# Kernel optimization log

Measured on AMD Instinct MI355X. Metric: run time of the kernel, lower is better.

Reference implementation:

```python
import jax, jax.numpy as jnp
import numpy as np

DIM_Q = 512
DIM_K = 512
DIM_V = 512
NUM_HEADS = 8
TEMPERATURE = 0.1
LN_EPS = 1e-5


def setup_inputs() -> dict:
    key = jax.random.key(0)
    ks = jax.random.split(key, 12)
    B, n_q, n_k = 8, 1024, 1024
    s = 0.02
    return {
        "Q": jax.random.normal(ks[0], (B, n_q, DIM_Q), jnp.float32),
        "K": jax.random.normal(ks[1], (B, n_k, DIM_K), jnp.float32),
        "mask": jnp.ones((B, n_k), dtype=bool),
        "Wq": jax.random.normal(ks[2], (DIM_Q, DIM_V), jnp.float32) * s,
        "bq": jnp.zeros((DIM_V,), jnp.float32),
        "Wk": jax.random.normal(ks[3], (DIM_K, DIM_V), jnp.float32) * s,
        "bk": jnp.zeros((DIM_V,), jnp.float32),
        "Wv": jax.random.normal(ks[4], (DIM_K, DIM_V), jnp.float32) * s,
        "bv": jnp.zeros((DIM_V,), jnp.float32),
        "Wo": jax.random.normal(ks[5], (DIM_V, DIM_V), jnp.float32) * s,
        "bo": jnp.zeros((DIM_V,), jnp.float32),
        "gamma": jnp.ones((DIM_V,), jnp.float32),
        "beta": jnp.zeros((DIM_V,), jnp.float32),
    }


def _mab(Q, K, mask, Wq, bq, Wk, bk, Wv, bv, Wo, bo, gamma, beta):
    B, n_q, _ = Q.shape
    n_k = K.shape[1]
    H = NUM_HEADS
    d_head = DIM_V // H
    # projections, split heads: [B, H, n, d_head]
    Qh = (Q @ Wq + bq).reshape(B, n_q, H, d_head).transpose(0, 2, 1, 3)
    Kh = (K @ Wk + bk).reshape(B, n_k, H, d_head).transpose(0, 2, 1, 3)
    Vh = (K @ Wv + bv).reshape(B, n_k, H, d_head).transpose(0, 2, 1, 3)
    scale = 1.0 / (np.sqrt(d_head) * TEMPERATURE)
    A = jnp.einsum("bhqd,bhkd->bhqk", Qh, Kh) * scale
    A = jnp.where(mask[:, None, None, :], A, -jnp.inf)
    A = jax.nn.softmax(A, axis=-1)
    O = jnp.einsum("bhqk,bhkd->bhqd", A, Vh)
    O = O.transpose(0, 2, 1, 3).reshape(B, n_q, DIM_V)
    # fused output FFN + residual + LN
    O = O + jax.nn.relu(O @ Wo + bo)
    mu = jnp.mean(O, axis=-1, keepdims=True)
    var = jnp.var(O, axis=-1, keepdims=True)
    return (O - mu) * jax.lax.rsqrt(var + LN_EPS) * gamma + beta


def reference(Q, K, mask, Wq, bq, Wk, bk, Wv, bv, Wo, bo, gamma, beta):
    return _mab(Q, K, mask, Wq, bq, Wk, bk, Wv, bv, Wo, bo, gamma, beta)
```

## Files before the change

### kernel.cpp

```cpp
#include <hip/hip_runtime.h>

typedef __bf16 bf16;
typedef bf16 bf16x4 __attribute__((ext_vector_type(4)));
typedef bf16 bf16x8 __attribute__((ext_vector_type(8)));
typedef float floatx4 __attribute__((ext_vector_type(4)));

#define NB 8
#define NQ 1024
#define NK 1024
#define DIM 512
#define NH 8
#define DH 64

__device__ __forceinline__ void async16(const void* g, void* l) {
    __builtin_amdgcn_global_load_lds(
        (const __attribute__((address_space(1))) unsigned int*)(unsigned long long)(g),
        (__attribute__((address_space(3))) unsigned int*)(unsigned long long)(l),
        16, 0, 0);
}

__global__ __launch_bounds__(256) void cast_kernel(
    const float* __restrict__ Q, const float* __restrict__ K,
    bf16* __restrict__ Qb, bf16* __restrict__ Kb)
{
    const int i = blockIdx.x * 256 + threadIdx.x;
    float4 a = ((const float4*)Q)[i];
    float4 c = ((const float4*)K)[i];
    bf16x4 qa = {(bf16)a.x, (bf16)a.y, (bf16)a.z, (bf16)a.w};
    bf16x4 ka = {(bf16)c.x, (bf16)c.y, (bf16)c.z, (bf16)c.w};
    *(bf16x4*)(Qb + (size_t)i * 4) = qa;
    *(bf16x4*)(Kb + (size_t)i * 4) = ka;
}

__global__ __launch_bounds__(256) void wtrans_kernel(
    const float* __restrict__ Wq, const float* __restrict__ Wk,
    const float* __restrict__ Wv, const float* __restrict__ Wo,
    bf16* __restrict__ Wt)
{
    const int w = blockIdx.z;
    const float* W = (w == 0) ? Wq : (w == 1) ? Wk : (w == 2) ? Wv : Wo;
    bf16* out = Wt + (size_t)w * DIM * DIM;
    const int k0 = blockIdx.x * 64, n0 = blockIdx.y * 64;
    __shared__ bf16 Tl[64][68];
    const int tx = threadIdx.x & 15, ty = threadIdx.x >> 4;
    for (int pass = 0; pass < 4; ++pass) {
        int k = ty + pass * 16;
        float4 v = *(const float4*)&W[(size_t)(k0 + k) * DIM + n0 + tx * 4];
        Tl[tx * 4 + 0][k] = (bf16)v.x;
        Tl[tx * 4 + 1][k] = (bf16)v.y;
        Tl[tx * 4 + 2][k] = (bf16)v.z;
        Tl[tx * 4 + 3][k] = (bf16)v.w;
    }
    __syncthreads();
    for (int pass = 0; pass < 4; ++pass) {
        int n = ty + pass * 16;
        bf16x4 ov = *(const bf16x4*)&Tl[n][tx * 4];
        *(bf16x4*)&out[(size_t)(n0 + n) * DIM + k0 + tx * 4] = ov;
    }
}

template<int MODE>
__global__ __launch_bounds__(256) void tile_gemm(
    const bf16* __restrict__ A, const bf16* __restrict__ W,
    const float* __restrict__ bias, const float* __restrict__ bias2,
    bf16* __restrict__ out, bf16* __restrict__ out2, float* __restrict__ yout)
{
    __shared__ __attribute__((aligned(16))) bf16 As[128 * 32];
    __shared__ __attribute__((aligned(16))) bf16 Bs[128 * 32];
    const int t = threadIdx.x;
    const int wave = t >> 6, lane = t & 63, quad = lane >> 4, l16 = lane & 15;
    const int wr = wave >> 1, wc = wave & 1;
    const int m0 = blockIdx.x * 128, n0 = blockIdx.y * 128;

    const int r1 = t >> 2, p1 = t & 3;
    const bf16* aSrc = A + (size_t)(m0 + r1) * DIM + p1 * 8;
    const bf16* wSrc = W + (size_t)(n0 + r1) * DIM + p1 * 8;
    bf16* aDst0 = As + t * 8;
    bf16* aDst1 = As + (t + 256) * 8;
    bf16* bDst0 = Bs + t * 8;
    bf16* bDst1 = Bs + (t + 256) * 8;

    floatx4 acc[4][4];
    for (int i = 0; i < 4; ++i)
        for (int j = 0; j < 4; ++j) acc[i][j] = (floatx4){0.f, 0.f, 0.f, 0.f};

    for (int kt = 0; kt < 16; ++kt) {
        __syncthreads();
        const int ko = kt * 32;
        async16(aSrc + ko, aDst0);
        async16(aSrc + 64 * DIM + ko, aDst1);
        async16(wSrc + ko, bDst0);
        async16(wSrc + 64 * DIM + ko, bDst1);
        __syncthreads();
        bf16x8 af[4], bfr[4];
        for (int mi = 0; mi < 4; ++mi)
            af[mi] = *(const bf16x8*)(As + (wr * 64 + mi * 16 + l16) * 32 + quad * 8);
        for (int ni = 0; ni < 4; ++ni)
            bfr[ni] = *(const bf16x8*)(Bs + (wc * 64 + ni * 16 + l16) * 32 + quad * 8);
        for (int mi = 0; mi < 4; ++mi)
            for (int ni = 0; ni < 4; ++ni)
                acc[mi][ni] = __builtin_amdgcn_mfma_f32_16x16x32_bf16(
                    af[mi], bfr[ni], acc[mi][ni], 0, 0, 0);
    }

    const bool isV = (MODE == 1) && (blockIdx.y >= 4);
    for (int ni = 0; ni < 4; ++ni) {
        const int n = n0 + wc * 64 + ni * 16 + l16;
        const float bb = isV ? bias2[n - 512] : bias[n];
        for (int mi = 0; mi < 4; ++mi) {
            for (int r = 0; r < 4; ++r) {
                const int m = m0 + wr * 64 + mi * 16 + quad * 4 + r;
                const float v = acc[mi][ni][r] + bb;
                if (MODE == 2) {
                    const float ov = (float)A[(size_t)m * DIM + n];
                    yout[(size_t)m * DIM + n] = ov + fmaxf(v, 0.f);
                } else if (!isV) {
                    const int b = m >> 10, q = m & 1023, h = n >> 6, d = n & 63;
                    out[((size_t)(b * 8 + h) * 1024 + q) * 64 + d] = (bf16)v;
                } else {
                    const int b = m >> 10, q = m & 1023;
                    const int nv = n - 512, h = nv >> 6, d = nv & 63;
                    out2[((size_t)(b * 8 + h) * 64 + d) * 1024 + q] = (bf16)v;
                }
            }
        }
    }
}

__global__ __launch_bounds__(256) void attn_kernel(
    const bf16* __restrict__ Qp, const bf16* __restrict__ Kp,
    const bf16* __restrict__ Vpt, const int* __restrict__ mask,
    bf16* __restrict__ Oa)
{
    const int bh = blockIdx.x & 63, qblk = blockIdx.x >> 6;
    const int b = bh >> 3, h = bh & 7;
    const int t = threadIdx.x;
    const int wave = t >> 6, lane = t & 63, quad = lane >> 4, l16 = lane & 15;
    const float scale = 1.25f;

    __shared__ __attribute__((aligned(16))) bf16 Kt[64 * 64];
    __shared__ __attribute__((aligned(16))) bf16 Vt[64 * 64];
    __shared__ __attribute__((aligned(16))) bf16 Pl[4][16][72];

    const bf16* Qbase = Qp + ((size_t)bh * NQ + qblk * 64 + wave * 16) * DH;
    const bf16* Kbase = Kp + (size_t)bh * NK * DH;
    const bf16* Vbase = Vpt + (size_t)bh * DH * NK;
    const int* mrow = mask + b * NK;

    bf16x8 qf0 = *(const bf16x8*)(Qbase + l16 * DH + quad * 8);
    bf16x8 qf1 = *(const bf16x8*)(Qbase + l16 * DH + 32 + quad * 8);

    floatx4 o[4];
    float lsum[4];
    for (int i = 0; i < 4; ++i) { o[i] = (floatx4){0.f, 0.f, 0.f, 0.f}; lsum[i] = 0.f; }

    const int r1 = t >> 3, s1 = t & 7;
    const int p1 = s1 ^ (r1 & 7);
    const bf16* kSrc = Kbase + r1 * 64 + p1 * 8;
    const bf16* vSrc = Vbase + (size_t)r1 * 1024 + p1 * 8;
    bf16* kDst0 = Kt + t * 8;
    bf16* kDst1 = Kt + (t + 256) * 8;
    bf16* vDst0 = Vt + t * 8;
    bf16* vDst1 = Vt + (t + 256) * 8;

    for (int kt = 0; kt < NK / 64; ++kt) {
        __syncthreads();
        async16(kSrc + kt * 4096, kDst0);
        async16(kSrc + kt * 4096 + 32 * 64, kDst1);
        async16(vSrc + kt * 64, vDst0);
        async16(vSrc + kt * 64 + (size_t)32 * 1024, vDst1);
        __syncthreads();

        floatx4 sf[4];
        for (int sub = 0; sub < 4; ++sub) {
            const int rowk = sub * 16 + l16;
            bf16x8 b0 = *(const bf16x8*)(Kt + rowk * 64 + ((quad ^ (rowk & 7)) << 3));
            bf16x8 b1 = *(const bf16x8*)(Kt + rowk * 64 + (((quad + 4) ^ (rowk & 7)) << 3));
            floatx4 s = {0.f, 0.f, 0.f, 0.f};
            s = __builtin_amdgcn_mfma_f32_16x16x32_bf16(qf0, b0, s, 0, 0, 0);
            s = __builtin_amdgcn_mfma_f32_16x16x32_bf16(qf1, b1, s, 0, 0, 0);
            sf[sub] = s;
        }
        for (int sub = 0; sub < 4; ++sub) {
            const int key = kt * 64 + sub * 16 + l16;
            const float madd = (mrow[key] != 0) ? 0.f : -3.0e38f;
            for (int r = 0; r < 4; ++r) {
                float p = __expf(sf[sub][r] * scale + madd);
                sf[sub][r] = p;
                lsum[r] += p;
            }
        }
        for (int sub = 0; sub < 4; ++sub)
            for (int r = 0; r < 4; ++r)
                Pl[wave][quad * 4 + r][sub * 16 + l16] = (bf16)sf[sub][r];
        bf16x8 af0 = *(const bf16x8*)&Pl[wave][l16][quad * 8];
        bf16x8 af1 = *(const bf16x8*)&Pl[wave][l16][32 + quad * 8];
        for (int dsub = 0; dsub < 4; ++dsub) {
            const int rowd = dsub * 16 + l16;
            bf16x8 b0 = *(const bf16x8*)(Vt + rowd * 64 + ((quad ^ (rowd & 7)) << 3));
            bf16x8 b1 = *(const bf16x8*)(Vt + rowd * 64 + (((quad + 4) ^ (rowd & 7)) << 3));
            o[dsub] = __builtin_amdgcn_mfma_f32_16x16x32_bf16(af0, b0, o[dsub], 0, 0, 0);
            o[dsub] = __builtin_amdgcn_mfma_f32_16x16x32_bf16(af1, b1, o[dsub], 0, 0, 0);
        }
    }

    float linv[4];
    for (int r = 0; r < 4; ++r) {
        float lr = lsum[r];
        lr += __shfl_xor(lr, 1, 64);
        lr += __shfl_xor(lr, 2, 64);
        lr += __shfl_xor(lr, 4, 64);
        lr += __shfl_xor(lr, 8, 64);
        linv[r] = 1.f / lr;
    }
    for (int dsub = 0; dsub < 4; ++dsub) {
        for (int r = 0; r < 4; ++r) {
            const int q = qblk * 64 + wave * 16 + quad * 4 + r;
            const int col = h * 64 + dsub * 16 + l16;
            Oa[((size_t)(b * NQ + q)) * DIM + col] = (bf16)(o[dsub][r] * linv[r]);
        }
    }
}

__global__ __launch_bounds__(256) void ln_kernel(
    const float* __restrict__ Y, const float* __restrict__ gamma,
    const float* __restrict__ beta, float* __restrict__ out)
{
    const int row  = blockIdx.x * 4 + (threadIdx.x >> 6);
    const int lane = threadIdx.x & 63;
    const float* y = Y + (size_t)row * DIM;
    float4 a = ((const float4*)y)[lane];
    float4 c = ((const float4*)y)[lane + 64];
    float s  = a.x + a.y + a.z + a.w + c.x + c.y + c.z + c.w;
    float sq = a.x*a.x + a.y*a.y + a.z*a.z + a.w*a.w
             + c.x*c.x + c.y*c.y + c.z*c.z + c.w*c.w;
    for (int mk = 32; mk >= 1; mk >>= 1) {
        s  += __shfl_xor(s,  mk, 64);
        sq += __shfl_xor(sq, mk, 64);
    }
    const float mu  = s * (1.f / 512.f);
    const float var = sq * (1.f / 512.f) - mu * mu;
    const float inv = rsqrtf(var + 1e-5f);
    float4 g1 = ((const float4*)gamma)[lane];
    float4 g2 = ((const float4*)gamma)[lane + 64];
    float4 b1 = ((const float4*)beta)[lane];
    float4 b2 = ((const float4*)beta)[lane + 64];
    float4 o1, o2;
    o1.x = (a.x - mu) * inv * g1.x + b1.x;
    o1.y = (a.y - mu) * inv * g1.y + b1.y;
    o1.z = (a.z - mu) * inv * g1.z + b1.z;
    o1.w = (a.w - mu) * inv * g1.w + b1.w;
    o2.x = (c.x - mu) * inv * g2.x + b2.x;
    o2.y = (c.y - mu) * inv * g2.y + b2.y;
    o2.z = (c.z - mu) * inv * g2.z + b2.z;
    o2.w = (c.w - mu) * inv * g2.w + b2.w;
    float* orow = out + (size_t)row * DIM;
    ((float4*)orow)[lane]      = o1;
    ((float4*)orow)[lane + 64] = o2;
}

extern "C" void kernel_launch(void* const* d_in, const int* in_sizes, int n_in,
                              void* d_out, int out_size, void* d_ws, size_t ws_size,
                              hipStream_t stream) {
    const float* Q  = (const float*)d_in[0];
    const float* K  = (const float*)d_in[1];
    const int*   mask = (const int*)d_in[2];
    const float* Wq = (const float*)d_in[3];
    const float* bq = (const float*)d_in[4];
    const float* Wk = (const float*)d_in[5];
    const float* bk = (const float*)d_in[6];
    const float* Wv = (const float*)d_in[7];
    const float* bv = (const float*)d_in[8];
    const float* Wo = (const float*)d_in[9];
    const float* bo = (const float*)d_in[10];
    const float* gamma = (const float*)d_in[11];
    const float* beta  = (const float*)d_in[12];

    char* ws = (char*)d_ws;
    bf16* Wt  = (bf16*)(ws);
    bf16* Qb  = (bf16*)(ws + 2097152);
    bf16* Kb  = (bf16*)(ws + 10485760);
    bf16* Qp  = (bf16*)(ws + 18874368);
    bf16* Kp  = (bf16*)(ws + 27262976);
    bf16* Vpt = (bf16*)(ws + 35651584);
    bf16* Oa  = (bf16*)(ws + 44040192);
    float* Yf = (float*)(ws + 52428800);
    float* out = (float*)d_out;

    cast_kernel<<<4096, 256, 0, stream>>>(Q, K, Qb, Kb);
    wtrans_kernel<<<dim3(8, 8, 4), 256, 0, stream>>>(Wq, Wk, Wv, Wo, Wt);
    tile_gemm<0><<<dim3(64, 4), 256, 0, stream>>>(Qb, Wt, bq, nullptr, Qp, nullptr, nullptr);
    tile_gemm<1><<<dim3(64, 8), 256, 0, stream>>>(Kb, Wt + 262144, bk, bv, Kp, Vpt, nullptr);
    attn_kernel<<<1024, 256, 0, stream>>>(Qp, Kp, Vpt, mask, Oa);
    tile_gemm<2><<<dim3(64, 4), 256, 0, stream>>>(Oa, Wt + 3 * 262144, bo, nullptr, nullptr, nullptr, Yf);
    ln_kernel<<<2048, 256, 0, stream>>>(Yf, gamma, beta, out);
}
```

Before: 192.5 us.

## Merge prep and projection launches, shrink GEMM tiles, widen attention query tiles

Merges the cast and weight-transpose kernels into one launch, and merges the Q and K/V projection GEMMs into one launch with 64x128 tiles. Each attention block now handles 128 queries, with each wave computing two 16-row groups that share K/V fragments. The FFN GEMM also moves to 64-row tiles so more blocks run. The goal is fewer launches, better CU fill for the GEMMs, and more reuse of K/V per block in attention. The cost is that attention runs half as many blocks (512) and holds more registers per wave, which may reduce occupancy.

```diff
diff --git a/kernel.cpp b/kernel.cpp
--- a/kernel.cpp
+++ b/kernel.cpp
@@ -19,108 +19,113 @@
         16, 0, 0);
 }
 
-__global__ __launch_bounds__(256) void cast_kernel(
+__global__ __launch_bounds__(256) void prep_fused(
     const float* __restrict__ Q, const float* __restrict__ K,
-    bf16* __restrict__ Qb, bf16* __restrict__ Kb)
-{
-    const int i = blockIdx.x * 256 + threadIdx.x;
-    float4 a = ((const float4*)Q)[i];
-    float4 c = ((const float4*)K)[i];
-    bf16x4 qa = {(bf16)a.x, (bf16)a.y, (bf16)a.z, (bf16)a.w};
-    bf16x4 ka = {(bf16)c.x, (bf16)c.y, (bf16)c.z, (bf16)c.w};
-    *(bf16x4*)(Qb + (size_t)i * 4) = qa;
-    *(bf16x4*)(Kb + (size_t)i * 4) = ka;
-}
-
-__global__ __launch_bounds__(256) void wtrans_kernel(
     const float* __restrict__ Wq, const float* __restrict__ Wk,
     const float* __restrict__ Wv, const float* __restrict__ Wo,
-    bf16* __restrict__ Wt)
-{
-    const int w = blockIdx.z;
-    const float* W = (w == 0) ? Wq : (w == 1) ? Wk : (w == 2) ? Wv : Wo;
-    bf16* out = Wt + (size_t)w * DIM * DIM;
-    const int k0 = blockIdx.x * 64, n0 = blockIdx.y * 64;
+    bf16* __restrict__ Qb, bf16* __restrict__ Kb, bf16* __restrict__ Wt)
+{
     __shared__ bf16 Tl[64][68];
-    const int tx = threadIdx.x & 15, ty = threadIdx.x >> 4;
-    for (int pass = 0; pass < 4; ++pass) {
-        int k = ty + pass * 16;
-        float4 v = *(const float4*)&W[(size_t)(k0 + k) * DIM + n0 + tx * 4];
-        Tl[tx * 4 + 0][k] = (bf16)v.x;
-        Tl[tx * 4 + 1][k] = (bf16)v.y;
-        Tl[tx * 4 + 2][k] = (bf16)v.z;
-        Tl[tx * 4 + 3][k] = (bf16)v.w;
-    }
-    __syncthreads();
-    for (int pass = 0; pass < 4; ++pass) {
-        int n = ty + pass * 16;
-        bf16x4 ov = *(const bf16x4*)&Tl[n][tx * 4];
-        *(bf16x4*)&out[(size_t)(n0 + n) * DIM + k0 + tx * 4] = ov;
-    }
-}
-
-template<int MODE>
-__global__ __launch_bounds__(256) void tile_gemm(
-    const bf16* __restrict__ A, const bf16* __restrict__ W,
-    const float* __restrict__ bias, const float* __restrict__ bias2,
-    bf16* __restrict__ out, bf16* __restrict__ out2, float* __restrict__ yout)
-{
-    __shared__ __attribute__((aligned(16))) bf16 As[128 * 32];
+    const int bid = blockIdx.x;
+    if (bid < 4096) {
+        const int i = bid * 256 + threadIdx.x;
+        float4 a = ((const float4*)Q)[i];
+        float4 c = ((const float4*)K)[i];
+        bf16x4 qa = {(bf16)a.x, (bf16)a.y, (bf16)a.z, (bf16)a.w};
+        bf16x4 ka = {(bf16)c.x, (bf16)c.y, (bf16)c.z, (bf16)c.w};
+        *(bf16x4*)(Qb + (size_t)i * 4) = qa;
+        *(bf16x4*)(Kb + (size_t)i * 4) = ka;
+    } else {
+        const int bid2 = bid - 4096;
+        const int w = bid2 >> 6;
+        const int bx = bid2 & 7, by = (bid2 >> 3) & 7;
+        const float* W = (w == 0) ? Wq : (w == 1) ? Wk : (w == 2) ? Wv : Wo;
+        bf16* out = Wt + (size_t)w * DIM * DIM;
+        const int k0 = bx * 64, n0 = by * 64;
+        const int tx = threadIdx.x & 15, ty = threadIdx.x >> 4;
+        for (int pass = 0; pass < 4; ++pass) {
+            int k = ty + pass * 16;
+            float4 v = *(const float4*)&W[(size_t)(k0 + k) * DIM + n0 + tx * 4];
+            Tl[tx * 4 + 0][k] = (bf16)v.x;
+            Tl[tx * 4 + 1][k] = (bf16)v.y;
+            Tl[tx * 4 + 2][k] = (bf16)v.z;
+            Tl[tx * 4 + 3][k] = (bf16)v.w;
+        }
+        __syncthreads();
+        for (int pass = 0; pass < 4; ++pass) {
+            int n = ty + pass * 16;
+            bf16x4 ov = *(const bf16x4*)&Tl[n][tx * 4];
+            *(bf16x4*)&out[(size_t)(n0 + n) * DIM + k0 + tx * 4] = ov;
+        }
+    }
+}
+
+__global__ __launch_bounds__(256) void proj_fused(
+    const bf16* __restrict__ Qb, const bf16* __restrict__ Kb,
+    const bf16* __restrict__ Wt,
+    const float* __restrict__ bq, const float* __restrict__ bk,
+    const float* __restrict__ bv,
+    bf16* __restrict__ Qp, bf16* __restrict__ Kp, bf16* __restrict__ Vpt)
+{
+    __shared__ __attribute__((aligned(16))) bf16 As[64 * 32];
     __shared__ __attribute__((aligned(16))) bf16 Bs[128 * 32];
     const int t = threadIdx.x;
     const int wave = t >> 6, lane = t & 63, quad = lane >> 4, l16 = lane & 15;
     const int wr = wave >> 1, wc = wave & 1;
-    const int m0 = blockIdx.x * 128, n0 = blockIdx.y * 128;
-
-    const int r1 = t >> 2, p1 = t & 3;
-    const bf16* aSrc = A + (size_t)(m0 + r1) * DIM + p1 * 8;
-    const bf16* wSrc = W + (size_t)(n0 + r1) * DIM + p1 * 8;
-    bf16* aDst0 = As + t * 8;
-    bf16* aDst1 = As + (t + 256) * 8;
+    const int bid = blockIdx.x;
+    const bool isQ = bid < 512;
+    const bf16* A; const bf16* W; int m0, n0;
+    if (isQ) { A = Qb; W = Wt;             m0 = (bid >> 2) * 64;  n0 = (bid & 3) * 128; }
+    else     { int b2 = bid - 512;
+               A = Kb; W = Wt + 512 * DIM; m0 = (b2 >> 3) * 64;   n0 = (b2 & 7) * 128; }
+
+    const bf16* aSrc = A + (size_t)(m0 + (t >> 2)) * DIM + (t & 3) * 8;
+    const bf16* wSrc = W + (size_t)(n0 + (t >> 2)) * DIM + (t & 3) * 8;
+    bf16* aDst  = As + t * 8;
     bf16* bDst0 = Bs + t * 8;
     bf16* bDst1 = Bs + (t + 256) * 8;
 
-    floatx4 acc[4][4];
-    for (int i = 0; i < 4; ++i)
+    floatx4 acc[2][4];
+    for (int i = 0; i < 2; ++i)
         for (int j = 0; j < 4; ++j) acc[i][j] = (floatx4){0.f, 0.f, 0.f, 0.f};
 
     for (int kt = 0; kt < 16; ++kt) {
         __syncthreads();
         const int ko = kt * 32;
-        async16(aSrc + ko, aDst0);
-        async16(aSrc + 64 * DIM + ko, aDst1);
+        async16(aSrc + ko, aDst);
         async16(wSrc + ko, bDst0);
         async16(wSrc + 64 * DIM + ko, bDst1);
         __syncthreads();
-        bf16x8 af[4], bfr[4];
-        for (int mi = 0; mi < 4; ++mi)
-            af[mi] = *(const bf16x8*)(As + (wr * 64 + mi * 16 + l16) * 32 + quad * 8);
+        bf16x8 af[2], bfr[4];
+        for (int mi = 0; mi < 2; ++mi)
+            af[mi] = *(const bf16x8*)(As + (wr * 32 + mi * 16 + l16) * 32 + quad * 8);
         for (int ni = 0; ni < 4; ++ni)
             bfr[ni] = *(const bf16x8*)(Bs + (wc * 64 + ni * 16 + l16) * 32 + quad * 8);
-        for (int mi = 0; mi < 4; ++mi)
+        for (int mi = 0; mi < 2; ++mi)
             for (int ni = 0; ni < 4; ++ni)
                 acc[mi][ni] = __builtin_amdgcn_mfma_f32_16x16x32_bf16(
                     af[mi], bfr[ni], acc[mi][ni], 0, 0, 0);
     }
 
-    const bool isV = (MODE == 1) && (blockIdx.y >= 4);
     for (int ni = 0; ni < 4; ++ni) {
         const int n = n0 + wc * 64 + ni * 16 + l16;
-        const float bb = isV ? bias2[n - 512] : bias[n];
-        for (int mi = 0; mi < 4; ++mi) {
+        float bb;
+        if (isQ) bb = bq[n];
+        else     bb = (n < 512) ? bk[n] : bv[n - 512];
+        for (int mi = 0; mi < 2; ++mi) {
             for (int r = 0; r < 4; ++r) {
-                const int m = m0 + wr * 64 + mi * 16 + quad * 4 + r;
+                const int m = m0 + wr * 32 + mi * 16 + quad * 4 + r;
                 const float v = acc[mi][ni][r] + bb;
-                if (MODE == 2) {
-                    const float ov = (float)A[(size_t)m * DIM + n];
-                    yout[(size_t)m * DIM + n] = ov + fmaxf(v, 0.f);
-                } else if (!isV) {
-                    const int b = m >> 10, q = m & 1023, h = n >> 6, d = n & 63;
-                    out[((size_t)(b * 8 + h) * 1024 + q) * 64 + d] = (bf16)v;
+                const int b = m >> 10, q = m & 1023;
+                if (isQ) {
+                    const int hd = n >> 6, d = n & 63;
+                    Qp[((size_t)(b * 8 + hd) * 1024 + q) * 64 + d] = (bf16)v;
+                } else if (n < 512) {
+                    const int hd = n >> 6, d = n & 63;
+                    Kp[((size_t)(b * 8 + hd) * 1024 + q) * 64 + d] = (bf16)v;
                 } else {
-                    const int b = m >> 10, q = m & 1023;
-                    const int nv = n - 512, h = nv >> 6, d = nv & 63;
-                    out2[((size_t)(b * 8 + h) * 64 + d) * 1024 + q] = (bf16)v;
+                    const int nv = n - 512, hd = nv >> 6, d = nv & 63;
+                    Vpt[((size_t)(b * 8 + hd) * 64 + d) * 1024 + q] = (bf16)v;
                 }
             }
         }
@@ -133,26 +138,29 @@
     bf16* __restrict__ Oa)
 {
     const int bh = blockIdx.x & 63, qblk = blockIdx.x >> 6;
-    const int b = bh >> 3, h = bh & 7;
+    const int b = bh >> 3, hd = bh & 7;
     const int t = threadIdx.x;
     const int wave = t >> 6, lane = t & 63, quad = lane >> 4, l16 = lane & 15;
     const float scale = 1.25f;
 
     __shared__ __attribute__((aligned(16))) bf16 Kt[64 * 64];
     __shared__ __attribute__((aligned(16))) bf16 Vt[64 * 64];
-    __shared__ __attribute__((aligned(16))) bf16 Pl[4][16][72];
-
-    const bf16* Qbase = Qp + ((size_t)bh * NQ + qblk * 64 + wave * 16) * DH;
+    __shared__ __attribute__((aligned(16))) bf16 Pl[4][32][72];
+
+    const bf16* Qbase = Qp + ((size_t)bh * NQ + qblk * 128 + wave * 32) * DH;
     const bf16* Kbase = Kp + (size_t)bh * NK * DH;
     const bf16* Vbase = Vpt + (size_t)bh * DH * NK;
     const int* mrow = mask + b * NK;
 
-    bf16x8 qf0 = *(const bf16x8*)(Qbase + l16 * DH + quad * 8);
-    bf16x8 qf1 = *(const bf16x8*)(Qbase + l16 * DH + 32 + quad * 8);
-
-    floatx4 o[4];
-    float lsum[4];
-    for (int i = 0; i < 4; ++i) { o[i] = (floatx4){0.f, 0.f, 0.f, 0.f}; lsum[i] = 0.f; }
+    bf16x8 qf[2][2];
+    for (int g = 0; g < 2; ++g)
+        for (int hh = 0; hh < 2; ++hh)
+            qf[g][hh] = *(const bf16x8*)(Qbase + (g * 16 + l16) * DH + hh * 32 + quad * 8);
+
+    floatx4 o[2][4];
+    float lsum[2][4];
+    for (int g = 0; g < 2; ++g)
+        for (int i = 0; i < 4; ++i) { o[g][i] = (floatx4){0.f,0.f,0.f,0.f}; lsum[g][i] = 0.f; }
 
     const int r1 = t >> 3, s1 = t & 7;
     const int p1 = s1 ^ (r1 & 7);
@@ -171,53 +179,118 @@
         async16(vSrc + kt * 64 + (size_t)32 * 1024, vDst1);
         __syncthreads();
 
-        floatx4 sf[4];
+        bf16x8 kb[4][2];
         for (int sub = 0; sub < 4; ++sub) {
             const int rowk = sub * 16 + l16;
-            bf16x8 b0 = *(const bf16x8*)(Kt + rowk * 64 + ((quad ^ (rowk & 7)) << 3));
-            bf16x8 b1 = *(const bf16x8*)(Kt + rowk * 64 + (((quad + 4) ^ (rowk & 7)) << 3));
-            floatx4 s = {0.f, 0.f, 0.f, 0.f};
-            s = __builtin_amdgcn_mfma_f32_16x16x32_bf16(qf0, b0, s, 0, 0, 0);
-            s = __builtin_amdgcn_mfma_f32_16x16x32_bf16(qf1, b1, s, 0, 0, 0);
-            sf[sub] = s;
-        }
+            kb[sub][0] = *(const bf16x8*)(Kt + rowk * 64 + ((quad ^ (rowk & 7)) << 3));
+            kb[sub][1] = *(const bf16x8*)(Kt + rowk * 64 + (((quad + 4) ^ (rowk & 7)) << 3));
+        }
+        floatx4 sf[2][4];
+        for (int g = 0; g < 2; ++g)
+            for (int sub = 0; sub < 4; ++sub) {
+                floatx4 s = {0.f, 0.f, 0.f, 0.f};
+                s = __builtin_amdgcn_mfma_f32_16x16x32_bf16(qf[g][0], kb[sub][0], s, 0, 0, 0);
+                s = __builtin_amdgcn_mfma_f32_16x16x32_bf16(qf[g][1], kb[sub][1], s, 0, 0, 0);
+                sf[g][sub] = s;
+            }
         for (int sub = 0; sub < 4; ++sub) {
             const int key = kt * 64 + sub * 16 + l16;
             const float madd = (mrow[key] != 0) ? 0.f : -3.0e38f;
-            for (int r = 0; r < 4; ++r) {
-                float p = __expf(sf[sub][r] * scale + madd);
-                sf[sub][r] = p;
-                lsum[r] += p;
-            }
-        }
-        for (int sub = 0; sub < 4; ++sub)
-            for (int r = 0; r < 4; ++r)
-                Pl[wave][quad * 4 + r][sub * 16 + l16] = (bf16)sf[sub][r];
-        bf16x8 af0 = *(const bf16x8*)&Pl[wave][l16][quad * 8];
-        bf16x8 af1 = *(const bf16x8*)&Pl[wave][l16][32 + quad * 8];
+            for (int g = 0; g < 2; ++g)
+                for (int r = 0; r < 4; ++r) {
+                    float p = __expf(sf[g][sub][r] * scale + madd);
+                    sf[g][sub][r] = p;
+                    lsum[g][r] += p;
+                }
+        }
+        for (int g = 0; g < 2; ++g)
+            for (int sub = 0; sub < 4; ++sub)
+                for (int r = 0; r < 4; ++r)
+                    Pl[wave][g * 16 + quad * 4 + r][sub * 16 + l16] = (bf16)sf[g][sub][r];
+        bf16x8 af[2][2];
+        for (int g = 0; g < 2; ++g)
+            for (int hh = 0; hh < 2; ++hh)
+                af[g][hh] = *(const bf16x8*)&Pl[wave][g * 16 + l16][hh * 32 + quad * 8];
         for (int dsub = 0; dsub < 4; ++dsub) {
             const int rowd = dsub * 16 + l16;
-            bf16x8 b0 = *(const bf16x8*)(Vt + rowd * 64 + ((quad ^ (rowd & 7)) << 3));
-            bf16x8 b1 = *(const bf16x8*)(Vt + rowd * 64 + (((quad + 4) ^ (rowd & 7)) << 3));
-            o[dsub] = __builtin_amdgcn_mfma_f32_16x16x32_bf16(af0, b0, o[dsub], 0, 0, 0);
-            o[dsub] = __builtin_amdgcn_mfma_f32_16x16x32_bf16(af1, b1, o[dsub], 0, 0, 0);
-        }
-    }
-
-    float linv[4];
-    for (int r = 0; r < 4; ++r) {
-        float lr = lsum[r];
-        lr += __shfl_xor(lr, 1, 64);
-        lr += __shfl_xor(lr, 2, 64);
-        lr += __shfl_xor(lr, 4, 64);
-        lr += __shfl_xor(lr, 8, 64);
-        linv[r] = 1.f / lr;
-    }
-    for (int dsub = 0; dsub < 4; ++dsub) {
+            bf16x8 v0 = *(const bf16x8*)(Vt + rowd * 64 + ((quad ^ (rowd & 7)) << 3));
+            bf16x8 v1 = *(const bf16x8*)(Vt + rowd * 64 + (((quad + 4) ^ (rowd & 7)) << 3));
+            for (int g = 0; g < 2; ++g) {
+                o[g][dsub] = __builtin_amdgcn_mfma_f32_16x16x32_bf16(af[g][0], v0, o[g][dsub], 0, 0, 0);
+                o[g][dsub] = __builtin_amdgcn_mfma_f32_16x16x32_bf16(af[g][1], v1, o[g][dsub], 0, 0, 0);
+            }
+        }
+    }
+
+    for (int g = 0; g < 2; ++g) {
+        float linv[4];
         for (int r = 0; r < 4; ++r) {
-            const int q = qblk * 64 + wave * 16 + quad * 4 + r;
-            const int col = h * 64 + dsub * 16 + l16;
-            Oa[((size_t)(b * NQ + q)) * DIM + col] = (bf16)(o[dsub][r] * linv[r]);
+            float lr = lsum[g][r];
+            lr += __shfl_xor(lr, 1, 64);
+            lr += __shfl_xor(lr, 2, 64);
+            lr += __shfl_xor(lr, 4, 64);
+            lr += __shfl_xor(lr, 8, 64);
+            linv[r] = 1.f / lr;
+        }
+        for (int dsub = 0; dsub < 4; ++dsub) {
+            for (int r = 0; r < 4; ++r) {
+                const int q = qblk * 128 + wave * 32 + g * 16 + quad * 4 + r;
+                const int col = hd * 64 + dsub * 16 + l16;
+                Oa[((size_t)(b * NQ + q)) * DIM + col] = (bf16)(o[g][dsub][r] * linv[r]);
+            }
+        }
+    }
+}
+
+__global__ __launch_bounds__(256) void ffn_gemm(
+    const bf16* __restrict__ Oa, const bf16* __restrict__ W,
+    const float* __restrict__ bias, float* __restrict__ Y)
+{
+    __shared__ __attribute__((aligned(16))) bf16 As[64 * 32];
+    __shared__ __attribute__((aligned(16))) bf16 Bs[128 * 32];
+    const int t = threadIdx.x;
+    const int wave = t >> 6, lane = t & 63, quad = lane >> 4, l16 = lane & 15;
+    const int wr = wave >> 1, wc = wave & 1;
+    const int m0 = (blockIdx.x >> 2) * 64, n0 = (blockIdx.x & 3) * 128;
+
+    const bf16* aSrc = Oa + (size_t)(m0 + (t >> 2)) * DIM + (t & 3) * 8;
+    const bf16* wSrc = W  + (size_t)(n0 + (t >> 2)) * DIM + (t & 3) * 8;
+    bf16* aDst  = As + t * 8;
+    bf16* bDst0 = Bs + t * 8;
+    bf16* bDst1 = Bs + (t + 256) * 8;
+
+    floatx4 acc[2][4];
+    for (int i = 0; i < 2; ++i)
+        for (int j = 0; j < 4; ++j) acc[i][j] = (floatx4){0.f, 0.f, 0.f, 0.f};
+
+    for (int kt = 0; kt < 16; ++kt) {
+        __syncthreads();
+        const int ko = kt * 32;
+        async16(aSrc + ko, aDst);
+        async16(wSrc + ko, bDst0);
+        async16(wSrc + 64 * DIM + ko, bDst1);
+        __syncthreads();
+        bf16x8 af[2], bfr[4];
+        for (int mi = 0; mi < 2; ++mi)
+            af[mi] = *(const bf16x8*)(As + (wr * 32 + mi * 16 + l16) * 32 + quad * 8);
+        for (int ni = 0; ni < 4; ++ni)
+            bfr[ni] = *(const bf16x8*)(Bs + (wc * 64 + ni * 16 + l16) * 32 + quad * 8);
+        for (int mi = 0; mi < 2; ++mi)
+            for (int ni = 0; ni < 4; ++ni)
+                acc[mi][ni] = __builtin_amdgcn_mfma_f32_16x16x32_bf16(
+                    af[mi], bfr[ni], acc[mi][ni], 0, 0, 0);
+    }
+
+    for (int ni = 0; ni < 4; ++ni) {
+        const int n = n0 + wc * 64 + ni * 16 + l16;
+        const float bb = bias[n];
+        for (int mi = 0; mi < 2; ++mi) {
+            for (int r = 0; r < 4; ++r) {
+                const int m = m0 + wr * 32 + mi * 16 + quad * 4 + r;
+                const float ov = (float)Oa[(size_t)m * DIM + n];
+                const float v = acc[mi][ni][r] + bb;
+                Y[(size_t)m * DIM + n] = ov + fmaxf(v, 0.f);
+            }
         }
     }
 }
@@ -287,11 +360,9 @@
     float* Yf = (float*)(ws + 52428800);
     float* out = (float*)d_out;
 
-    cast_kernel<<<4096, 256, 0, stream>>>(Q, K, Qb, Kb);
-    wtrans_kernel<<<dim3(8, 8, 4), 256, 0, stream>>>(Wq, Wk, Wv, Wo, Wt);
-    tile_gemm<0><<<dim3(64, 4), 256, 0, stream>>>(Qb, Wt, bq, nullptr, Qp, nullptr, nullptr);
-    tile_gemm<1><<<dim3(64, 8), 256, 0, stream>>>(Kb, Wt + 262144, bk, bv, Kp, Vpt, nullptr);
-    attn_kernel<<<1024, 256, 0, stream>>>(Qp, Kp, Vpt, mask, Oa);
-    tile_gemm<2><<<dim3(64, 4), 256, 0, stream>>>(Oa, Wt + 3 * 262144, bo, nullptr, nullptr, nullptr, Yf);
+    prep_fused<<<4352, 256, 0, stream>>>(Q, K, Wq, Wk, Wv, Wo, Qb, Kb, Wt);
+    proj_fused<<<1536, 256, 0, stream>>>(Qb, Kb, Wt, bq, bk, bv, Qp, Kp, Vpt);
+    attn_kernel<<<512, 256, 0, stream>>>(Qp, Kp, Vpt, mask, Oa);
+    ffn_gemm<<<512, 256, 0, stream>>>(Oa, Wt + 3 * 262144, bo, Yf);
     ln_kernel<<<2048, 256, 0, stream>>>(Yf, gamma, beta, out);
 }
```

Result: slower. 202.4 us (+5.1%).
